# Optimization experiments

Hardware: AMD Instinct MI355X
Metric: run time of the kernel (lower is better)

Reference implementation:

```python
import math
import jax, jax.numpy as jnp
import numpy as np

ANCHORS = np.array([[10,13],[16,30],[33,23],[30,61],[62,45],[59,119],[116,90],[156,198],[373,326]], dtype=np.float32)
NUM_CLASSES = 80
INPUT_SHAPE = (416, 416)
ANCHORS_MASK = [[6,7,8],[3,4,5],[0,1,2]]
IGNORE_THR = 0.5
BALANCE = [0.4, 1.0, 4.0]
BOX_RATIO = 0.05
OBJ_RATIO = 5.0 * (INPUT_SHAPE[0] * INPUT_SHAPE[1]) / 416.0**2
CLS_RATIO = NUM_CLASSES / 80.0


def _bce_logits(x, t):
    # BCEWithLogitsLoss(reduction='none'): softplus(x) - t*x (numerically stable)
    return jnp.logaddexp(0.0, x) - x * t


def _get_target(targets, anchors, in_w, in_h):
    # targets: [B, N, 5] = [class, cx, cy, w, h] normalized; anchors: [3, 2] (scaled units)
    B, N = targets.shape[:2]
    A = anchors.shape[0]
    cls = targets[..., 0].astype(jnp.int32)                       # [B,N]
    gx = targets[..., 1] * in_w
    gy = targets[..., 2] * in_h
    gwh = targets[..., 3:5] * jnp.array([in_w, in_h], jnp.float32)  # [B,N,2] grid units (unit mismatch kept on purpose)
    inter = jnp.minimum(gwh[:, :, None, :], anchors[None, None, :, :]).prod(-1)  # [B,N,A]
    anchor_iou = inter / (gwh.prod(-1)[..., None] + anchors.prod(-1)[None, None, :] - inter + 1e-6)
    best_n = jnp.argmax(anchor_iou, axis=-1)                       # [B,N]
    gi = jnp.floor(gx).astype(jnp.int32)                           # cx in (0,1) -> always < in_w
    gj = jnp.floor(gy).astype(jnp.int32)
    b_idx = jnp.broadcast_to(jnp.arange(B)[:, None], (B, N))

    zeros = jnp.zeros((B, A, in_h, in_w), jnp.float32)
    noobj = jnp.ones((B, A, in_h, in_w), jnp.float32)
    # zero noobj at (gj,gi) for every anchor with iou > thr (scatter-min == set 0)
    noobj = noobj.at[b_idx[:, :, None], jnp.arange(A)[None, None, :], gj[:, :, None], gi[:, :, None]].min(
        jnp.where(anchor_iou > IGNORE_THR, 0.0, 1.0))
    noobj = noobj.at[b_idx, best_n, gj, gi].min(0.0)
    mask = zeros.at[b_idx, best_n, gj, gi].max(1.0)
    tx = zeros.at[b_idx, best_n, gj, gi].set(gx - gi)
    ty = zeros.at[b_idx, best_n, gj, gi].set(gy - gj)
    tw = zeros.at[b_idx, best_n, gj, gi].set(jnp.log(gwh[..., 0] / anchors[best_n, 0]))
    th = zeros.at[b_idx, best_n, gj, gi].set(jnp.log(gwh[..., 1] / anchors[best_n, 1]))
    t_cls = jnp.zeros((B, A, in_h, in_w, NUM_CLASSES), jnp.float32).at[b_idx, best_n, gj, gi, cls].set(1.0)
    bls = zeros.at[b_idx, best_n, gj, gi].set(2.0 - targets[..., 3] * targets[..., 4])
    return mask, noobj, tx, ty, tw, th, t_cls, bls


def _bbox_ciou(b1, b2):
    # b1, b2: [..., 4] in xywh
    b1x1, b1y1 = b1[..., 0] - b1[..., 2] / 2, b1[..., 1] - b1[..., 3] / 2
    b1x2, b1y2 = b1[..., 0] + b1[..., 2] / 2, b1[..., 1] + b1[..., 3] / 2
    b2x1, b2y1 = b2[..., 0] - b2[..., 2] / 2, b2[..., 1] - b2[..., 3] / 2
    b2x2, b2y2 = b2[..., 0] + b2[..., 2] / 2, b2[..., 1] + b2[..., 3] / 2
    area1 = b1[..., 2] * b1[..., 3]
    area2 = b2[..., 2] * b2[..., 3]
    iw = jnp.clip(jnp.minimum(b1x2, b2x2) - jnp.maximum(b1x1, b2x1), 0.0)
    ih = jnp.clip(jnp.minimum(b1y2, b2y2) - jnp.maximum(b1y1, b2y1), 0.0)
    inter = iw * ih
    iou = inter / (area1 + area2 - inter + 1e-6)
    d2 = (b2[..., 0] - b1[..., 0]) ** 2 + (b2[..., 1] - b1[..., 1]) ** 2
    c2 = (jnp.maximum(b1x2, b2x2) - jnp.minimum(b1x1, b2x1)) ** 2 + \
         (jnp.maximum(b1y2, b2y2) - jnp.minimum(b1y1, b2y1)) ** 2 + 1e-6
    v = 4.0 * (jnp.arctan(b1[..., 2] / (b1[..., 3] + 1e-6)) - jnp.arctan(b2[..., 2] / (b2[..., 3] + 1e-6))) ** 2 / math.pi ** 2
    alpha = jax.lax.stop_gradient(v / (1.0 - iou + v + 1e-6))
    return iou - d2 / c2 - alpha * v


def _yolo_loss(l_prediction, m_prediction, s_prediction, targets):
    targets = jax.lax.stop_gradient(targets)
    scaled_anchors = jnp.asarray(ANCHORS) / jnp.array([INPUT_SHAPE[1], INPUT_SHAPE[0]], jnp.float32)
    loss_box = 0.0
    loss_conf = 0.0
    loss_cls = 0.0
    for i, pred in enumerate([l_prediction, m_prediction, s_prediction]):
        B, A, H, W = pred.shape[:4]
        anchors = scaled_anchors[jnp.array(ANCHORS_MASK[i])]        # [3,2]
        dx = jax.nn.sigmoid(pred[..., 0])
        dy = jax.nn.sigmoid(pred[..., 1])
        dw = pred[..., 2]
        dh = pred[..., 3]
        conf = pred[..., 4]
        pcls = pred[..., 5:]
        tgt = jax.lax.stop_gradient(_get_target(targets, anchors, W, H))
        mask, noobj, tx, ty, tw, th, t_cls, bls = tgt
        gx = jnp.broadcast_to(jnp.arange(W, dtype=jnp.float32)[None, None, None, :], (B, A, H, W))
        gy = jnp.broadcast_to(jnp.arange(H, dtype=jnp.float32)[None, None, :, None], (B, A, H, W))
        aw = jnp.broadcast_to(anchors[:, 0][None, :, None, None], (B, A, H, W))
        ah = jnp.broadcast_to(anchors[:, 1][None, :, None, None], (B, A, H, W))
        pred_bbox = jnp.stack([dx + gx, dy + gy, jnp.exp(dw) * aw, jnp.exp(dh) * ah], axis=-1)
        target_bbox = jnp.stack([tx + gx, ty + gy, jnp.exp(tw) * aw, jnp.exp(th) * ah], axis=-1)
        ciou = _bbox_ciou(pred_bbox, target_bbox)
        loss_box = loss_box + jnp.sum(mask * (1.0 - ciou) * bls)
        loss_conf = loss_conf + BALANCE[i] * (jnp.sum(mask * _bce_logits(conf, 1.0)) +
                                              jnp.sum(noobj * _bce_logits(conf, 0.0)))
        loss_cls = loss_cls + jnp.sum(mask[..., None] * _bce_logits(pcls, t_cls))
    return BOX_RATIO * loss_box + OBJ_RATIO * loss_conf + CLS_RATIO * loss_cls


def setup_inputs() -> dict:
    key = jax.random.key(0)
    k1, k2, k3, k4, k5, k6 = jax.random.split(key, 6)
    B, N = 32, 50
    l_prediction = jax.random.normal(k1, (B, 3, 13, 13, 5 + NUM_CLASSES), jnp.float32)
    m_prediction = jax.random.normal(k2, (B, 3, 26, 26, 5 + NUM_CLASSES), jnp.float32)
    s_prediction = jax.random.normal(k3, (B, 3, 52, 52, 5 + NUM_CLASSES), jnp.float32)
    cls = jax.random.randint(k4, (B, N, 1), 0, NUM_CLASSES).astype(jnp.float32)
    cxy = jax.random.uniform(k5, (B, N, 2), jnp.float32, 0.01, 0.99)
    wh = jax.random.uniform(k6, (B, N, 2), jnp.float32, 0.02, 0.45)
    targets = jnp.concatenate([cls, cxy, wh], axis=-1)  # [B, N, 5]
    return {"l_prediction": l_prediction, "m_prediction": m_prediction,
            "s_prediction": s_prediction, "targets": targets}


def reference(l_prediction, m_prediction, s_prediction, targets):
    return _yolo_loss(l_prediction, m_prediction, s_prediction, targets)
```

## Files before the change

kernel.cpp:

```cpp
#include <hip/hip_runtime.h>
#include <math.h>


__constant__ float c_anch[9][2] = {
    {10.f, 13.f},  {16.f, 30.f},   {33.f, 23.f},
    {30.f, 61.f},  {62.f, 45.f},   {59.f, 119.f},
    {116.f, 90.f}, {156.f, 198.f}, {373.f, 326.f}};

__device__ __forceinline__ float sp_fast(float x) {
  return fmaxf(x, 0.f) + __logf(1.f + __expf(-fabsf(x)));
}
__device__ __forceinline__ float sigmoid_fast(float x) {
  return 1.f / (1.f + __expf(-x));
}

__device__ __forceinline__ float ciou_f(float px, float py, float pw, float ph,
                                        float gx, float gy, float gw, float gh) {
  float p_x1 = px - pw * 0.5f, p_x2 = px + pw * 0.5f;
  float p_y1 = py - ph * 0.5f, p_y2 = py + ph * 0.5f;
  float g_x1 = gx - gw * 0.5f, g_x2 = gx + gw * 0.5f;
  float g_y1 = gy - gh * 0.5f, g_y2 = gy + gh * 0.5f;
  float iw = fmaxf(fminf(p_x2, g_x2) - fmaxf(p_x1, g_x1), 0.f);
  float ih = fmaxf(fminf(p_y2, g_y2) - fmaxf(p_y1, g_y1), 0.f);
  float inter = iw * ih;
  float a1 = pw * ph, a2 = gw * gh;
  float iou = inter / (a1 + a2 - inter + 1e-6f);
  float dx = gx - px, dy = gy - py;
  float d2 = dx * dx + dy * dy;
  float cw = fmaxf(p_x2, g_x2) - fminf(p_x1, g_x1);
  float ch = fmaxf(p_y2, g_y2) - fminf(p_y1, g_y1);
  float c2 = cw * cw + ch * ch + 1e-6f;
  float dv = atanf(pw / (ph + 1e-6f)) - atanf(gw / (gh + 1e-6f));
  float v = 0.4052847346f * dv * dv;
  float alpha = v / (1.f - iou + v + 1e-6f);
  return iou - d2 / c2 - alpha * v;
}

__global__ __launch_bounds__(256) void yolo_fused(
    const float* __restrict__ predL, const float* __restrict__ predM,
    const float* __restrict__ predS, const float* __restrict__ targets,
    float* __restrict__ partial) {
  __shared__ int skey[150];
  __shared__ float spay[150][5];
  __shared__ float wsum[4];
  const int b = blockIdx.y;
  const int t = threadIdx.x;

  if (t < 150) {
    int s = t / 50;
    int n = t - s * 50;
    const float* tg = targets + (b * 50 + n) * 5;
    float cls = tg[0], cx = tg[1], cy = tg[2], w = tg[3], h = tg[4];
    float Wf = (float)(13 << s);
    float gx = cx * Wf, gy = cy * Wf, gw = w * Wf, gh = h * Wf;
    float areag = gw * gh;
    float best = -1.f;
    int bn = 0, ign = 0;
    for (int k = 0; k < 3; ++k) {
      float aw = c_anch[(2 - s) * 3 + k][0] * (1.f / 416.f);
      float ah = c_anch[(2 - s) * 3 + k][1] * (1.f / 416.f);
      float inter = fminf(gw, aw) * fminf(gh, ah);
      float iou = inter / (areag + aw * ah - inter + 1e-6f);
      if (iou > best) { best = iou; bn = k; }
      if (iou > 0.5f) ign |= (1 << k);
    }
    int gi = (int)floorf(gx);
    int gj = (int)floorf(gy);
    skey[t] = gi | (gj << 6) | (bn << 12) | (ign << 14) | (((int)cls) << 17);
    spay[t][0] = gx; spay[t][1] = gy; spay[t][2] = gw; spay[t][3] = gh;
    spay[t][4] = 2.f - w * h;
  }
  __syncthreads();

  int cell = blockIdx.x * 256 + t;
  float local = 0.f;
  if (cell < 10647) {
    int s, c;
    const float* pred;
    if (cell < 507)        { s = 0; c = cell;        pred = predL; }
    else if (cell < 2535)  { s = 1; c = cell - 507;  pred = predM; }
    else                   { s = 2; c = cell - 2535; pred = predS; }
    const int W = 13 << s;
    const int HW = W * W;
    int a = (c >> (2 * s)) / 169;
    int rem = c - a * HW;
    int j = (rem >> s) / 13;
    int i = rem - j * W;
    const float* pc = pred + (size_t)((b * 3 + a) * HW + rem) * 85;
    float conf = pc[4];

    int probe = i | (j << 6);
    int m = -1;
    bool ign = false;
    const int base = s * 50;
    for (int n = 0; n < 50; ++n) {
      int k = skey[base + n];
      if ((k & 0xFFF) == probe) {
        if (((k >> 12) & 3) == a) m = base + n;
        ign = ign || (((k >> (14 + a)) & 1) != 0);
      }
    }
    float BAL = (s == 0) ? 0.4f : ((s == 1) ? 1.0f : 4.0f);
    if (m >= 0) {
      local += 5.f * BAL * (sp_fast(conf) - conf);
      float aw = c_anch[(2 - s) * 3 + a][0] * (1.f / 416.f);
      float ah = c_anch[(2 - s) * 3 + a][1] * (1.f / 416.f);
      float px = sigmoid_fast(pc[0]) + (float)i;
      float py = sigmoid_fast(pc[1]) + (float)j;
      float pw = __expf(pc[2]) * aw;
      float ph = __expf(pc[3]) * ah;
      float ci = ciou_f(px, py, pw, ph, spay[m][0], spay[m][1], spay[m][2],
                        spay[m][3]);
      local += 0.05f * (1.f - ci) * spay[m][4];
      int clsi = (skey[m] >> 17) & 0x7F;
      float cs = 0.f;
#pragma unroll 4
      for (int cch = 0; cch < 80; ++cch) cs += sp_fast(pc[5 + cch]);
      cs -= pc[5 + clsi];
      local += cs;
    } else if (!ign) {
      local += 5.f * BAL * sp_fast(conf);
    }
  }

#pragma unroll
  for (int off = 32; off > 0; off >>= 1) local += __shfl_down(local, off, 64);
  int lane = t & 63, wid = t >> 6;
  if (lane == 0) wsum[wid] = local;
  __syncthreads();
  if (t == 0)
    partial[b * gridDim.x + blockIdx.x] = wsum[0] + wsum[1] + wsum[2] + wsum[3];
}

__global__ __launch_bounds__(256) void reduce_kernel(
    const float* __restrict__ partial, float* __restrict__ out, int n) {
  __shared__ float wsum[4];
  float v = 0.f;
  for (int idx = threadIdx.x; idx < n; idx += 256) v += partial[idx];
#pragma unroll
  for (int off = 32; off > 0; off >>= 1) v += __shfl_down(v, off, 64);
  int lane = threadIdx.x & 63, wid = threadIdx.x >> 6;
  if (lane == 0) wsum[wid] = v;
  __syncthreads();
  if (threadIdx.x == 0) out[0] = wsum[0] + wsum[1] + wsum[2] + wsum[3];
}

extern "C" void kernel_launch(void* const* d_in, const int* in_sizes, int n_in,
                              void* d_out, int out_size, void* d_ws,
                              size_t ws_size, hipStream_t stream) {
  const float* l = (const float*)d_in[0];
  const float* m = (const float*)d_in[1];
  const float* s = (const float*)d_in[2];
  const float* tg = (const float*)d_in[3];
  float* out = (float*)d_out;
  float* partial = (float*)d_ws;

  hipLaunchKernelGGL(yolo_fused, dim3(42, 32), dim3(256), 0, stream, l, m, s,
                     tg, partial);
  hipLaunchKernelGGL(reduce_kernel, dim3(1), dim3(256), 0, stream, partial,
                     out, 42 * 32);
}
```

Baseline: 157.5 us.

## Offload matched-cell box and class loss to dedicated wavefront-parallel blocks

Splits the fused kernel into two block roles. The original 42 blocks per image now compute only the objectness loss per cell. Four extra blocks per image handle the per-target box and class loss, with one wavefront per target reading the 85-channel row coalesced across lanes and reducing with shuffles, using a ballot to deduplicate targets that hit the same cell and anchor. This removes the serial 80-iteration class loop from a single thread, which caused heavy divergence and uncoalesced loads, at the cost of recomputing target digests per wavefront and launching more blocks.

```diff
diff --git a/kernel.cpp b/kernel.cpp
--- a/kernel.cpp
+++ b/kernel.cpp
@@ -28,12 +28,35 @@
   float dx = gx - px, dy = gy - py;
   float d2 = dx * dx + dy * dy;
   float cw = fmaxf(p_x2, g_x2) - fminf(p_x1, g_x1);
-  float ch = fmaxf(p_y2, g_y2) - fminf(p_y1, g_y1);
-  float c2 = cw * cw + ch * ch + 1e-6f;
+  float chh = fmaxf(p_y2, g_y2) - fminf(p_y1, g_y1);
+  float c2 = cw * cw + chh * chh + 1e-6f;
   float dv = atanf(pw / (ph + 1e-6f)) - atanf(gw / (gh + 1e-6f));
   float v = 0.4052847346f * dv * dv;
   float alpha = v / (1.f - iou + v + 1e-6f);
   return iou - d2 / c2 - alpha * v;
+}
+
+__device__ __forceinline__ int digest(float cx, float cy, float w, float h,
+                                      int s, float* gx, float* gy, float* gw,
+                                      float* gh) {
+  float Wf = (float)(13 << s);
+  float x = cx * Wf, y = cy * Wf, ww = w * Wf, hh = h * Wf;
+  float areag = ww * hh;
+  float best = -1.f;
+  int bn = 0, ign = 0;
+#pragma unroll
+  for (int k = 0; k < 3; ++k) {
+    float aw = c_anch[(2 - s) * 3 + k][0] * (1.f / 416.f);
+    float ah = c_anch[(2 - s) * 3 + k][1] * (1.f / 416.f);
+    float inter = fminf(ww, aw) * fminf(hh, ah);
+    float iou = inter / (areag + aw * ah - inter + 1e-6f);
+    if (iou > best) { best = iou; bn = k; }
+    if (iou > 0.5f) ign |= (1 << k);
+  }
+  int gi = (int)floorf(x);
+  int gj = (int)floorf(y);
+  *gx = x; *gy = y; *gw = ww; *gh = hh;
+  return gi | (gj << 6) | (bn << 12) | (ign << 14);
 }
 
 __global__ __launch_bounds__(256) void yolo_fused(
@@ -41,91 +64,106 @@
     const float* __restrict__ predS, const float* __restrict__ targets,
     float* __restrict__ partial) {
   __shared__ int skey[150];
-  __shared__ float spay[150][5];
   __shared__ float wsum[4];
   const int b = blockIdx.y;
   const int t = threadIdx.x;
-
-  if (t < 150) {
-    int s = t / 50;
-    int n = t - s * 50;
-    const float* tg = targets + (b * 50 + n) * 5;
-    float cls = tg[0], cx = tg[1], cy = tg[2], w = tg[3], h = tg[4];
-    float Wf = (float)(13 << s);
-    float gx = cx * Wf, gy = cy * Wf, gw = w * Wf, gh = h * Wf;
-    float areag = gw * gh;
-    float best = -1.f;
-    int bn = 0, ign = 0;
-    for (int k = 0; k < 3; ++k) {
-      float aw = c_anch[(2 - s) * 3 + k][0] * (1.f / 416.f);
-      float ah = c_anch[(2 - s) * 3 + k][1] * (1.f / 416.f);
-      float inter = fminf(gw, aw) * fminf(gh, ah);
-      float iou = inter / (areag + aw * ah - inter + 1e-6f);
-      if (iou > best) { best = iou; bn = k; }
-      if (iou > 0.5f) ign |= (1 << k);
-    }
-    int gi = (int)floorf(gx);
-    int gj = (int)floorf(gy);
-    skey[t] = gi | (gj << 6) | (bn << 12) | (ign << 14) | (((int)cls) << 17);
-    spay[t][0] = gx; spay[t][1] = gy; spay[t][2] = gw; spay[t][3] = gh;
-    spay[t][4] = 2.f - w * h;
+  const int lane = t & 63, wid = t >> 6;
+  float local = 0.f;
+
+  if (blockIdx.x < 42) {
+    if (t < 150) {
+      int s = t / 50;
+      int n = t - s * 50;
+      const float* tg = targets + (b * 50 + n) * 5;
+      float gx, gy, gw, gh;
+      skey[t] = digest(tg[1], tg[2], tg[3], tg[4], s, &gx, &gy, &gw, &gh);
+    }
+    __syncthreads();
+
+    int cell = blockIdx.x * 256 + t;
+    if (cell < 10647) {
+      int s, c;
+      const float* pred;
+      if (cell < 507)       { s = 0; c = cell;        pred = predL; }
+      else if (cell < 2535) { s = 1; c = cell - 507;  pred = predM; }
+      else                  { s = 2; c = cell - 2535; pred = predS; }
+      const int W = 13 << s;
+      const int HW = W * W;
+      int a = (c >> (2 * s)) / 169;
+      int rem = c - a * HW;
+      int j = (rem >> s) / 13;
+      int i = rem - j * W;
+      float conf = pred[(size_t)((b * 3 + a) * HW + rem) * 85 + 4];
+
+      int probe = i | (j << 6);
+      bool masked = false, ign = false;
+      const int base = s * 50;
+      for (int n = 0; n < 50; ++n) {
+        int k = skey[base + n];
+        if ((k & 0xFFF) == probe) {
+          masked = masked || (((k >> 12) & 3) == a);
+          ign = ign || (((k >> (14 + a)) & 1) != 0);
+        }
+      }
+      float BAL = (s == 0) ? 0.4f : ((s == 1) ? 1.0f : 4.0f);
+      if (masked)
+        local = 5.f * BAL * (sp_fast(conf) - conf);
+      else if (!ign)
+        local = 5.f * BAL * sp_fast(conf);
+    }
+  } else {
+    const int wglob = (blockIdx.x - 42) * 4 + wid;
+    float cls = 0.f, cx = 0.f, cy = 0.f, w = 0.f, h = 0.f;
+    if (lane < 50) {
+      const float* tg = targets + (b * 50 + lane) * 5;
+      cls = tg[0]; cx = tg[1]; cy = tg[2]; w = tg[3]; h = tg[4];
+    }
+    for (int task = wglob; task < 150; task += 16) {
+      int s = task / 50;
+      int n = task - s * 50;
+      int key = 0x7FFFFFFF;
+      float gx = 0.f, gy = 0.f, gw = 0.f, gh = 0.f;
+      if (lane < 50) key = digest(cx, cy, w, h, s, &gx, &gy, &gw, &gh);
+      int key_n = __shfl(key, n, 64);
+      unsigned long long later = __ballot(
+          lane < 50 && lane > n && ((key ^ key_n) & 0x3FFF) == 0);
+      if (later == 0ULL) {
+        float gxn = __shfl(gx, n, 64), gyn = __shfl(gy, n, 64);
+        float gwn = __shfl(gw, n, 64), ghn = __shfl(gh, n, 64);
+        float blsn = 2.f - __shfl(w, n, 64) * __shfl(h, n, 64);
+        int clsn = (int)__shfl(cls, n, 64);
+        int gi = key_n & 63, gj = (key_n >> 6) & 63, a = (key_n >> 12) & 3;
+        const float* pred = (s == 0) ? predL : ((s == 1) ? predM : predS);
+        const int W = 13 << s;
+        const int HW = W * W;
+        const float* pc = pred + (size_t)((b * 3 + a) * HW + gj * W + gi) * 85;
+        float c1 = pc[lane];
+        float c2 = (lane < 21) ? pc[64 + lane] : 0.f;
+        float v = (lane >= 5) ? sp_fast(c1) : 0.f;
+        if (lane < 21) v += sp_fast(c2);
+#pragma unroll
+        for (int off = 32; off > 0; off >>= 1) v += __shfl_down(v, off, 64);
+        int ch = 5 + clsn;
+        float pch = (ch < 64) ? __shfl(c1, ch, 64) : __shfl(c2, ch - 64, 64);
+        float p0 = __shfl(c1, 0, 64), p1 = __shfl(c1, 1, 64);
+        float p2 = __shfl(c1, 2, 64), p3 = __shfl(c1, 3, 64);
+        if (lane == 0) {
+          float aw = c_anch[(2 - s) * 3 + a][0] * (1.f / 416.f);
+          float ah = c_anch[(2 - s) * 3 + a][1] * (1.f / 416.f);
+          float px = sigmoid_fast(p0) + (float)gi;
+          float py = sigmoid_fast(p1) + (float)gj;
+          float pw = __expf(p2) * aw;
+          float ph = __expf(p3) * ah;
+          float ci = ciou_f(px, py, pw, ph, gxn, gyn, gwn, ghn);
+          local += (v - pch) + 0.05f * (1.f - ci) * blsn;
+        }
+      }
+    }
+    __syncthreads();
   }
-  __syncthreads();
-
-  int cell = blockIdx.x * 256 + t;
-  float local = 0.f;
-  if (cell < 10647) {
-    int s, c;
-    const float* pred;
-    if (cell < 507)        { s = 0; c = cell;        pred = predL; }
-    else if (cell < 2535)  { s = 1; c = cell - 507;  pred = predM; }
-    else                   { s = 2; c = cell - 2535; pred = predS; }
-    const int W = 13 << s;
-    const int HW = W * W;
-    int a = (c >> (2 * s)) / 169;
-    int rem = c - a * HW;
-    int j = (rem >> s) / 13;
-    int i = rem - j * W;
-    const float* pc = pred + (size_t)((b * 3 + a) * HW + rem) * 85;
-    float conf = pc[4];
-
-    int probe = i | (j << 6);
-    int m = -1;
-    bool ign = false;
-    const int base = s * 50;
-    for (int n = 0; n < 50; ++n) {
-      int k = skey[base + n];
-      if ((k & 0xFFF) == probe) {
-        if (((k >> 12) & 3) == a) m = base + n;
-        ign = ign || (((k >> (14 + a)) & 1) != 0);
-      }
-    }
-    float BAL = (s == 0) ? 0.4f : ((s == 1) ? 1.0f : 4.0f);
-    if (m >= 0) {
-      local += 5.f * BAL * (sp_fast(conf) - conf);
-      float aw = c_anch[(2 - s) * 3 + a][0] * (1.f / 416.f);
-      float ah = c_anch[(2 - s) * 3 + a][1] * (1.f / 416.f);
-      float px = sigmoid_fast(pc[0]) + (float)i;
-      float py = sigmoid_fast(pc[1]) + (float)j;
-      float pw = __expf(pc[2]) * aw;
-      float ph = __expf(pc[3]) * ah;
-      float ci = ciou_f(px, py, pw, ph, spay[m][0], spay[m][1], spay[m][2],
-                        spay[m][3]);
-      local += 0.05f * (1.f - ci) * spay[m][4];
-      int clsi = (skey[m] >> 17) & 0x7F;
-      float cs = 0.f;
-#pragma unroll 4
-      for (int cch = 0; cch < 80; ++cch) cs += sp_fast(pc[5 + cch]);
-      cs -= pc[5 + clsi];
-      local += cs;
-    } else if (!ign) {
-      local += 5.f * BAL * sp_fast(conf);
-    }
-  }
 
 #pragma unroll
   for (int off = 32; off > 0; off >>= 1) local += __shfl_down(local, off, 64);
-  int lane = t & 63, wid = t >> 6;
   if (lane == 0) wsum[wid] = local;
   __syncthreads();
   if (t == 0)
@@ -155,8 +193,8 @@
   float* out = (float*)d_out;
   float* partial = (float*)d_ws;
 
-  hipLaunchKernelGGL(yolo_fused, dim3(42, 32), dim3(256), 0, stream, l, m, s,
+  hipLaunchKernelGGL(yolo_fused, dim3(46, 32), dim3(256), 0, stream, l, m, s,
                      tg, partial);
   hipLaunchKernelGGL(reduce_kernel, dim3(1), dim3(256), 0, stream, partial,
-                     out, 42 * 32);
-}
+                     out, 46 * 32);
+}
```

New measurement: 158.8 us (median of 2 runs). No clear change (+0.9%).
